# Optimization experiments

Measured on AMD Instinct MI355X. Metric: run time of the kernel, lower is better.

The kernel has to match this reference:

```python
import jax, jax.numpy as jnp
import numpy as np

EPS = 1e-8


def setup_inputs() -> dict:
    key = jax.random.key(0)
    k1, k2, k3, k4 = jax.random.split(key, 4)
    b, cin, cout, H, W, ksz = 8, 512, 512, 64, 64, 3
    return {
        "x": jax.random.normal(k1, (b, cin, H, W), dtype=jnp.float32),
        "style": jax.random.normal(k2, (b, cin), dtype=jnp.float32),
        "noise": jax.random.normal(k3, (b, 1, H, W), dtype=jnp.float32),
        "weight": jax.random.normal(k4, (cout, cin, ksz, ksz), dtype=jnp.float32),
        "bias": jnp.zeros((1, cout, 1, 1), dtype=jnp.float32),
        "noise_strength": jnp.zeros((), dtype=jnp.float32),
    }


def reference(x, style, noise, weight, bias, noise_strength):
    cout, cin, k, _ = weight.shape
    b, _, H, W = x.shape
    scale = (1.0 / (cin * k * k)) ** 0.5

    # weight scaled and normalized by per-filter inf-norm
    w = weight * scale / jnp.max(jnp.abs(weight), axis=(1, 2, 3), keepdims=True)
    # style normalized by per-sample inf-norm
    s = style / jnp.max(jnp.abs(style), axis=1, keepdims=True)

    # modulate: (b, cout, cin, k, k)
    w = w[None] * s[:, None, :, None, None]
    # demodulate
    demod = jnp.sqrt(jnp.sum(w * w, axis=(2, 3, 4)) + EPS)  # (b, cout)
    w = w / demod[:, :, None, None, None]

    # grouped conv: one group per sample (note: input is scaled again, as in source)
    xr = (x * scale).reshape(1, b * cin, H, W)
    wr = w.reshape(b * cout, cin, k, k)
    out = jax.lax.conv_general_dilated(
        xr, wr, window_strides=(1, 1), padding=((1, 1), (1, 1)),
        dimension_numbers=("NCHW", "OIHW", "NCHW"), feature_group_count=b)
    out = out.reshape(b, cout, H, W) + bias
    out = out + noise * noise_strength
    return out
```

## Files before the change

kernel.cpp:

```cpp
#include <hip/hip_runtime.h>


#define EPSV   1e-8f
#define SCALEV 0.014731391274719738f

typedef __attribute__((ext_vector_type(8))) short short8;
typedef __attribute__((ext_vector_type(4))) float floatx4;

__device__ __forceinline__ void gload_lds16(const void* g, void* l) {
    __builtin_amdgcn_global_load_lds(
        (const __attribute__((address_space(1))) void*)g,
        (__attribute__((address_space(3))) void*)l, 16, 0, 0);
}

__device__ __forceinline__ unsigned short f2bf(float f) {
    unsigned u = __float_as_uint(f);
    unsigned r = (u + 0x7fffu + ((u >> 16) & 1u)) >> 16;
    return (unsigned short)r;
}

__global__ __launch_bounds__(256) void zero_ws(uint4* __restrict__ p, int n4) {
    uint4 z = {0u, 0u, 0u, 0u};
    int stride = gridDim.x * 256;
    for (int i = blockIdx.x * 256 + threadIdx.x; i < n4; i += stride) p[i] = z;
}

__global__ __launch_bounds__(512) void prep_style(
    const float* __restrict__ style, float* __restrict__ tbuf)
{
    const int b = blockIdx.x, t = threadIdx.x;
    float v = style[b * 512 + t];
    __shared__ float red[512];
    red[t] = fabsf(v);
    __syncthreads();
    for (int s = 256; s > 0; s >>= 1) {
        if (t < s) red[t] = fmaxf(red[t], red[t + s]);
        __syncthreads();
    }
    tbuf[b * 512 + t] = v / red[0];
}

__global__ __launch_bounds__(256) void prep_w(
    const float* __restrict__ weight, float* __restrict__ wsqn,
    unsigned short* __restrict__ Aw)
{
    const int co = blockIdx.x, t = threadIdx.x;
    const float* wp = weight + (size_t)co * 4608;
    float m = 0.f;
    for (int i = t; i < 4608; i += 256) m = fmaxf(m, fabsf(wp[i]));
    __shared__ float red[256];
    red[t] = m;
    __syncthreads();
    for (int s = 128; s > 0; s >>= 1) {
        if (t < s) red[t] = fmaxf(red[t], red[t + s]);
        __syncthreads();
    }
    const float inv = 1.f / red[0];
    for (int ci = t; ci < 512; ci += 256) {
        float s = 0.f;
        #pragma unroll
        for (int k = 0; k < 9; ++k) {
            float v = wp[ci * 9 + k] * inv;
            s = fmaf(v, v, s);
            Aw[(size_t)(co * 9 + k) * 512 + ci] = f2bf(v);
        }
        wsqn[co * 512 + ci] = s;
    }
}

__global__ __launch_bounds__(256) void prep_x(
    const float* __restrict__ x, const float* __restrict__ tbuf,
    unsigned short* __restrict__ xbp)
{
    const int cic = blockIdx.x;
    const int h   = blockIdx.y;
    const int b   = blockIdx.z;
    const int tid = threadIdx.x;
    __shared__ float tr[64][33];

    const int cl = tid >> 3;
    const int w0 = (tid & 7) << 3;
    const int ci = cic * 32 + cl;
    const float tv = tbuf[b * 512 + ci];
    const float* xp = x + (((size_t)(b * 512 + ci)) << 12) + (h << 6) + w0;
    float4 u = *(const float4*)xp;
    float4 v = *(const float4*)(xp + 4);
    tr[w0 + 0][cl] = u.x * tv; tr[w0 + 1][cl] = u.y * tv;
    tr[w0 + 2][cl] = u.z * tv; tr[w0 + 3][cl] = u.w * tv;
    tr[w0 + 4][cl] = v.x * tv; tr[w0 + 5][cl] = v.y * tv;
    tr[w0 + 6][cl] = v.z * tv; tr[w0 + 7][cl] = v.w * tv;
    __syncthreads();

    const int w  = tid >> 2;
    const int c8 = (tid & 3) << 3;
    unsigned short o[8] __attribute__((aligned(16)));
    #pragma unroll
    for (int j = 0; j < 8; ++j) o[j] = f2bf(tr[w][c8 + j]);
    size_t dst = ((size_t)((b * 66 + h + 1) * 66) + (w + 1)) * 512 + cic * 32 + c8;
    *(uint4*)&xbp[dst] = *(const uint4*)o;
}

__global__ __launch_bounds__(256) void gcoef(
    const float* __restrict__ wsqn, const float* __restrict__ tbuf,
    float* __restrict__ gbuf)
{
    const int b    = blockIdx.y;
    const int co   = blockIdx.x * 4 + (threadIdx.x >> 6);
    const int lane = threadIdx.x & 63;
    float sum = 0.f;
    for (int ci = lane; ci < 512; ci += 64) {
        float tv = tbuf[b * 512 + ci];
        sum = fmaf(tv * tv, wsqn[co * 512 + ci], sum);
    }
    #pragma unroll
    for (int off = 32; off > 0; off >>= 1) sum += __shfl_down(sum, off);
    if (lane == 0)
        gbuf[b * 512 + co] = SCALEV * SCALEV / sqrtf(fmaf(SCALEV * SCALEV, sum, EPSV));
}

__global__ __launch_bounds__(256, 2) void conv_mfma(
    const unsigned short* __restrict__ xbp, const unsigned short* __restrict__ Aw,
    const float* __restrict__ gbuf, const float* __restrict__ bias,
    const float* __restrict__ noise, const float* __restrict__ nstr,
    float* __restrict__ out)
{
    __shared__ __align__(16) short sA[2][4096];
    __shared__ __align__(16) short sB[2][6656];

    const int tid  = threadIdx.x;
    const int lane = tid & 63;
    const int wv   = tid >> 6;
    const int b    = blockIdx.z;
    const int co0  = blockIdx.y << 7;
    const int h0   = (blockIdx.x >> 1) << 2;
    const int w0   = (blockIdx.x & 1) << 5;

    const int n0  = lane & 15;
    const int kq  = lane >> 4;
    const int wco = (wv >> 1) << 6;
    const int wpx = (wv & 1) << 6;

    int prow[4], pcol[4], aoff[4];
    #pragma unroll
    for (int fj = 0; fj < 4; ++fj) {
        int p = wpx + fj * 16 + n0;
        prow[fj] = p >> 5;
        pcol[fj] = p & 31;
    }
    #pragma unroll
    for (int fi = 0; fi < 4; ++fi) aoff[fi] = (wco + fi * 16 + n0) * 32 + kq * 8;

    const int sl_px = lane >> 2;
    const int sl_ci = (lane & 3) << 3;

    floatx4 zz = {0.f, 0.f, 0.f, 0.f};
    floatx4 acc[4][4];
    #pragma unroll
    for (int i = 0; i < 4; ++i)
        #pragma unroll
        for (int j = 0; j < 4; ++j) acc[i][j] = zz;

    const unsigned short* xb = xbp + (size_t)b * 4356 * 512;

    for (int ci0 = 0; ci0 < 512; ci0 += 64) {
        __syncthreads();
        #pragma unroll
        for (int hf = 0; hf < 2; ++hf) {
            const unsigned short* src = xb + ci0 + hf * 32 + sl_ci;
            for (int j = wv; j < 13; j += 4) {
                int px = j * 16 + sl_px;
                if (px > 203) px = 203;
                int row = px / 34;
                int col = px - row * 34;
                gload_lds16(src + (((size_t)(h0 + row) * 66 + w0 + col) << 9),
                            &sB[hf][j * 512]);
            }
        }
        #pragma unroll 1
        for (int pos = 0; pos < 9; ++pos) {
            const int kh = pos / 3;
            const int kw = pos - kh * 3;
            if (pos) __syncthreads();
            #pragma unroll
            for (int hf = 0; hf < 2; ++hf) {
                for (int j = wv; j < 8; j += 4) {
                    int co = j * 16 + sl_px;
                    gload_lds16(Aw + (size_t)((co0 + co) * 9 + pos) * 512
                                   + ci0 + hf * 32 + sl_ci,
                                &sA[hf][j * 512]);
                }
            }
            __syncthreads();
            #pragma unroll
            for (int hf = 0; hf < 2; ++hf) {
                short8 af[4], bfr[4];
                #pragma unroll
                for (int fi = 0; fi < 4; ++fi)
                    af[fi] = *(const short8*)&sA[hf][aoff[fi]];
                #pragma unroll
                for (int fj = 0; fj < 4; ++fj)
                    bfr[fj] = *(const short8*)
                        &sB[hf][((prow[fj] + kh) * 34 + pcol[fj] + kw) * 32 + kq * 8];
                #pragma unroll
                for (int fi = 0; fi < 4; ++fi)
                    #pragma unroll
                    for (int fj = 0; fj < 4; ++fj)
                        acc[fi][fj] = __builtin_amdgcn_mfma_f32_16x16x32_bf16(
                            af[fi], bfr[fj], acc[fi][fj], 0, 0, 0);
            }
        }
    }

    const float ns = nstr[0];
    float nz[4];
    int ph[4], pw[4];
    #pragma unroll
    for (int fj = 0; fj < 4; ++fj) {
        int p = wpx + fj * 16 + n0;
        ph[fj] = h0 + (p >> 5);
        pw[fj] = w0 + (p & 31);
        nz[fj] = noise[(b << 12) + (ph[fj] << 6) + pw[fj]] * ns;
    }
    #pragma unroll
    for (int fi = 0; fi < 4; ++fi) {
        #pragma unroll
        for (int i = 0; i < 4; ++i) {
            int co = co0 + wco + fi * 16 + kq * 4 + i;
            float gg = gbuf[(b << 9) + co];
            float bb = bias[co];
            #pragma unroll
            for (int fj = 0; fj < 4; ++fj) {
                out[(((size_t)((b << 9) + co)) << 12) + (ph[fj] << 6) + pw[fj]] =
                    fmaf(gg, acc[fi][fj][i], bb + nz[fj]);
            }
        }
    }
}

extern "C" void kernel_launch(void* const* d_in, const int* in_sizes, int n_in,
                              void* d_out, int out_size, void* d_ws, size_t ws_size,
                              hipStream_t stream)
{
    const float* x      = (const float*)d_in[0];
    const float* style  = (const float*)d_in[1];
    const float* noise  = (const float*)d_in[2];
    const float* weight = (const float*)d_in[3];
    const float* bias   = (const float*)d_in[4];
    const float* nstr   = (const float*)d_in[5];
    float* out = (float*)d_out;
    char* ws = (char*)d_ws;

    float*          tbuf = (float*)(ws);
    float*          gbuf = (float*)(ws + 16384);
    float*          wsqn = (float*)(ws + 32768);
    unsigned short* Aw   = (unsigned short*)(ws + 1081344);
    unsigned short* xbp  = (unsigned short*)(ws + 5799936);

    hipLaunchKernelGGL(zero_ws, dim3(2048), dim3(256), 0, stream,
                       (uint4*)xbp, 35684352 / 16);
    hipLaunchKernelGGL(prep_style, dim3(8), dim3(512), 0, stream, style, tbuf);
    hipLaunchKernelGGL(prep_w, dim3(512), dim3(256), 0, stream, weight, wsqn, Aw);
    hipLaunchKernelGGL(prep_x, dim3(16, 64, 8), dim3(256), 0, stream, x, tbuf, xbp);
    hipLaunchKernelGGL(gcoef, dim3(128, 8), dim3(256), 0, stream, wsqn, tbuf, gbuf);
    hipLaunchKernelGGL(conv_mfma, dim3(32, 4, 8), dim3(256), 0, stream,
                       xbp, Aw, gbuf, bias, noise, nstr, out);
}
```

Before: 318.8 us.

## Swizzle LDS tiles to avoid bank conflicts and zero only padded borders

```diff
diff --git a/kernel.cpp b/kernel.cpp
--- a/kernel.cpp
+++ b/kernel.cpp
@@ -19,10 +19,18 @@
     return (unsigned short)r;
 }
 
-__global__ __launch_bounds__(256) void zero_ws(uint4* __restrict__ p, int n4) {
+__global__ __launch_bounds__(256) void zero_border(uint4* __restrict__ xbp4) {
+    int idx = blockIdx.x * 256 + threadIdx.x;
+    if (idx >= 133120) return;
+    int q    = idx & 63;
+    int cell = (idx >> 6) % 260;
+    int b    = idx / 16640;
+    int h, w;
+    if (cell < 66)       { h = 0;  w = cell; }
+    else if (cell < 132) { h = 65; w = cell - 66; }
+    else { int e = cell - 132; h = 1 + (e >> 1); w = (e & 1) * 65; }
     uint4 z = {0u, 0u, 0u, 0u};
-    int stride = gridDim.x * 256;
-    for (int i = blockIdx.x * 256 + threadIdx.x; i < n4; i += stride) p[i] = z;
+    xbp4[(size_t)((b * 66 + h) * 66 + w) * 64 + q] = z;
 }
 
 __global__ __launch_bounds__(512) void prep_style(
@@ -140,18 +148,20 @@
     const int wco = (wv >> 1) << 6;
     const int wpx = (wv & 1) << 6;
 
-    int prow[4], pcol[4], aoff[4];
+    int pb[4], aoff[4];
     #pragma unroll
     for (int fj = 0; fj < 4; ++fj) {
         int p = wpx + fj * 16 + n0;
-        prow[fj] = p >> 5;
-        pcol[fj] = p & 31;
-    }
-    #pragma unroll
-    for (int fi = 0; fi < 4; ++fi) aoff[fi] = (wco + fi * 16 + n0) * 32 + kq * 8;
+        pb[fj] = (p >> 5) * 34 + (p & 31);
+    }
+    #pragma unroll
+    for (int fi = 0; fi < 4; ++fi) {
+        int row = wco + fi * 16 + n0;
+        aoff[fi] = row * 32 + (((kq ^ (n0 >> 1)) & 3) << 3);
+    }
 
     const int sl_px = lane >> 2;
-    const int sl_ci = (lane & 3) << 3;
+    const int sw_ci = (((lane & 3) ^ (sl_px >> 1)) & 3) << 3;
 
     floatx4 zz = {0.f, 0.f, 0.f, 0.f};
     floatx4 acc[4][4];
@@ -166,7 +176,7 @@
         __syncthreads();
         #pragma unroll
         for (int hf = 0; hf < 2; ++hf) {
-            const unsigned short* src = xb + ci0 + hf * 32 + sl_ci;
+            const unsigned short* src = xb + ci0 + hf * 32 + sw_ci;
             for (int j = wv; j < 13; j += 4) {
                 int px = j * 16 + sl_px;
                 if (px > 203) px = 203;
@@ -186,11 +196,12 @@
                 for (int j = wv; j < 8; j += 4) {
                     int co = j * 16 + sl_px;
                     gload_lds16(Aw + (size_t)((co0 + co) * 9 + pos) * 512
-                                   + ci0 + hf * 32 + sl_ci,
+                                   + ci0 + hf * 32 + sw_ci,
                                 &sA[hf][j * 512]);
                 }
             }
             __syncthreads();
+            const int dpos = kh * 34 + kw;
             #pragma unroll
             for (int hf = 0; hf < 2; ++hf) {
                 short8 af[4], bfr[4];
@@ -198,9 +209,11 @@
                 for (int fi = 0; fi < 4; ++fi)
                     af[fi] = *(const short8*)&sA[hf][aoff[fi]];
                 #pragma unroll
-                for (int fj = 0; fj < 4; ++fj)
+                for (int fj = 0; fj < 4; ++fj) {
+                    int pr = pb[fj] + dpos;
                     bfr[fj] = *(const short8*)
-                        &sB[hf][((prow[fj] + kh) * 34 + pcol[fj] + kw) * 32 + kq * 8];
+                        &sB[hf][pr * 32 + (((kq ^ (pr >> 1)) & 3) << 3)];
+                }
                 #pragma unroll
                 for (int fi = 0; fi < 4; ++fi)
                     #pragma unroll
@@ -256,8 +269,7 @@
     unsigned short* Aw   = (unsigned short*)(ws + 1081344);
     unsigned short* xbp  = (unsigned short*)(ws + 5799936);
 
-    hipLaunchKernelGGL(zero_ws, dim3(2048), dim3(256), 0, stream,
-                       (uint4*)xbp, 35684352 / 16);
+    hipLaunchKernelGGL(zero_border, dim3(520), dim3(256), 0, stream, (uint4*)xbp);
     hipLaunchKernelGGL(prep_style, dim3(8), dim3(512), 0, stream, style, tbuf);
     hipLaunchKernelGGL(prep_w, dim3(512), dim3(256), 0, stream, weight, wsqn, Aw);
     hipLaunchKernelGGL(prep_x, dim3(16, 64, 8), dim3(256), 0, stream, x, tbuf, xbp);
```

New measurement: 302.1 us. 1.06x faster.
